# Kernel optimization log

Measured on AMD Instinct MI355X. Metric: run time of the kernel, lower is better.

## Reference

```python
import jax, jax.numpy as jnp
import numpy as np

B, T, C, H = 4, 2048, 1024, 16
D = C // H  # head_dim = 64
ROPE_BASE = 10000.0


def _rope_cos_sin(T, D, dtype):
    # inv_freq: (D/2,), freqs: (T, D/2) -> cos/sin tiled to (T, D)
    inv_freq = 1.0 / (ROPE_BASE ** (jnp.arange(0, D, 2, dtype=jnp.float32) / D))
    freqs = jnp.arange(T, dtype=jnp.float32)[:, None] * inv_freq[None, :]
    emb = jnp.concatenate([freqs, freqs], axis=-1)  # (T, D)
    return jnp.cos(emb).astype(dtype), jnp.sin(emb).astype(dtype)


def _rotate_half(x):
    x1, x2 = jnp.split(x, 2, axis=-1)
    return jnp.concatenate([-x2, x1], axis=-1)


def setup_inputs() -> dict:
    key = jax.random.key(0)
    k1, k2, k3 = jax.random.split(key, 3)
    x = jax.random.normal(k1, (B, T, C), dtype=jnp.float32)
    W_qkv = jax.random.normal(k2, (C, 3 * C), dtype=jnp.float32) * (C ** -0.5)
    b_qkv = jnp.zeros((3 * C,), dtype=jnp.float32)
    W_out = jax.random.normal(k3, (C, C), dtype=jnp.float32) * (C ** -0.5)
    b_out = jnp.zeros((C,), dtype=jnp.float32)
    return {"x": x, "W_qkv": W_qkv, "b_qkv": b_qkv, "W_out": W_out, "b_out": b_out}


def reference(x, W_qkv, b_qkv, W_out, b_out):
    Bx, Tx, Cx = x.shape
    qkv = x @ W_qkv + b_qkv                                   # (B, T, 3C)
    qkv = qkv.reshape(Bx, Tx, 3, H, D).transpose(2, 0, 3, 1, 4)  # (3, B, H, T, D)
    q, k, v = qkv[0], qkv[1], qkv[2]

    cos, sin = _rope_cos_sin(Tx, D, x.dtype)                  # (T, D) each
    q = q * cos + _rotate_half(q) * sin
    k = k * cos + _rotate_half(k) * sin

    # NOTE: original code has no 1/sqrt(D) scaling — faithful reproduction.
    att = jnp.einsum('bhtd,bhsd->bhts', q, k)                 # (B, H, T, T)
    causal = jnp.tril(jnp.ones((Tx, Tx), dtype=bool))
    att = jnp.where(causal[None, None, :, :], att, -jnp.inf)
    att = jax.nn.softmax(att, axis=-1)
    y = jnp.einsum('bhts,bhsd->bhtd', att, v)                 # (B, H, T, D)
    y = y.transpose(0, 2, 1, 3).reshape(Bx, Tx, Cx)
    return y @ W_out + b_out
```

## Files before the change

kernel.cpp:

```cpp
#include <hip/hip_runtime.h>
#include <math.h>

#define NB    4
#define T_SEQ 2048
#define CDIM  1024
#define NH    16
#define DH    64
#define NQKV  3072

typedef short bf16x8 __attribute__((ext_vector_type(8)));
typedef float f32x4  __attribute__((ext_vector_type(4)));

#define GLOBAL_AS __attribute__((address_space(1)))
#define LDS_AS    __attribute__((address_space(3)))

__device__ __forceinline__ void async16(const void* g, void* l) {
  __builtin_amdgcn_global_load_lds((const GLOBAL_AS void*)g, (LDS_AS void*)l, 16, 0, 0);
}

__device__ __forceinline__ unsigned short f2bf(float f) {
  unsigned u = __float_as_uint(f);
  unsigned r = u + 0x7FFF + ((u >> 16) & 1);
  return (unsigned short)(r >> 16);
}

#define SWZ8(row, c) ((((row) << 3) | ((c) ^ ((row) & 7))) << 3)

#define BARRIER()  asm volatile("s_barrier" ::: "memory")
#define VMCNT(n)   asm volatile("s_waitcnt vmcnt(" #n ")" ::: "memory")

__global__ __launch_bounds__(256) void rope_table(float2* __restrict__ tab) {
  int i = blockIdx.x * 256 + threadIdx.x;
  int t = i >> 5, d = i & 31;
  float inv = expf((float)d * -0.28782313662425572f);
  float s, c;
  sincosf((float)t * inv, &s, &c);
  tab[i] = make_float2(c, s);
}

__global__ __launch_bounds__(256) void convert_bf16(
    const float* __restrict__ in, unsigned short* __restrict__ out, int n4) {
  int i = blockIdx.x * 256 + threadIdx.x;
  if (i >= n4) return;
  float4 v = ((const float4*)in)[i];
  ushort4 o;
  o.x = f2bf(v.x); o.y = f2bf(v.y); o.z = f2bf(v.z); o.w = f2bf(v.w);
  ((ushort4*)out)[i] = o;
}

__global__ __launch_bounds__(256) void transpose_to_bf16(
    const float* __restrict__ in, unsigned short* __restrict__ out, int K, int N) {
  __shared__ float tile[32][33];
  int n0 = blockIdx.x << 5, k0 = blockIdx.y << 5;
  int r  = threadIdx.x >> 3;
  int c4 = (threadIdx.x & 7) << 2;
  float4 v = *(const float4*)&in[(size_t)(k0 + r) * N + n0 + c4];
  tile[r][c4 + 0] = v.x; tile[r][c4 + 1] = v.y;
  tile[r][c4 + 2] = v.z; tile[r][c4 + 3] = v.w;
  __syncthreads();
  ushort4 o;
  o.x = f2bf(tile[c4 + 0][r]); o.y = f2bf(tile[c4 + 1][r]);
  o.z = f2bf(tile[c4 + 2][r]); o.w = f2bf(tile[c4 + 3][r]);
  *(ushort4*)&out[(size_t)(n0 + r) * K + k0 + c4] = o;
}

__global__ __launch_bounds__(256) void transpose_v(
    const unsigned short* __restrict__ v, unsigned short* __restrict__ vt) {
  __shared__ unsigned short tile[64][65];
  int bh = blockIdx.y;
  int t0 = blockIdx.x << 6;
  size_t ib = (size_t)bh * (T_SEQ * DH);
  int tid = threadIdx.x;
#pragma unroll
  for (int u = 0; u < 2; ++u) {
    int f = u * 256 + tid;
    int tr = f >> 3, c = f & 7;
    bf16x8 val = *(const bf16x8*)&v[ib + (size_t)(t0 + tr) * DH + c * 8];
#pragma unroll
    for (int j = 0; j < 8; ++j) tile[tr][c * 8 + j] = (unsigned short)val[j];
  }
  __syncthreads();
#pragma unroll
  for (int u = 0; u < 2; ++u) {
    int f = u * 256 + tid;
    int d = f >> 3, c = f & 7;
    bf16x8 o;
#pragma unroll
    for (int j = 0; j < 8; ++j) o[j] = (short)tile[c * 8 + j][d];
    *(bf16x8*)&vt[ib + (size_t)d * T_SEQ + t0 + c * 8] = o;
  }
}

#define STAGE(kt, b)                                                          \
  { const unsigned short* sa_ = aSrc + (kt) * 64;                             \
    const unsigned short* sb_ = bSrc + (kt) * 64;                             \
    async16(sa_,          &As[b][d0]);                                        \
    async16(sa_ + 65536,  &As[b][d0 + 4096]);                                 \
    async16(sb_,          &Bs[b][d0]);                                        \
    async16(sb_ + 65536,  &Bs[b][d0 + 4096]);                                 \
    async16(sb_ + 131072, &Bs[b][d0 + 8192]);                                 \
    async16(sb_ + 196608, &Bs[b][d0 + 12288]); }

#define GEMM_PIPE(Aptr, Btptr)                                                \
  int tid = threadIdx.x;                                                      \
  int wave = tid >> 6, lane = tid & 63;                                       \
  int wm = wave >> 2, wn = wave & 3;                                          \
  int col = lane & 15, quad = lane >> 4;                                      \
  int srow = tid >> 3;                                                        \
  int schunk = (tid & 7) ^ (srow & 7);                                        \
  const unsigned short* aSrc = &Aptr[(size_t)(m0 + srow) * CDIM + schunk * 8];\
  const unsigned short* bSrc = &Btptr[(size_t)(n0 + srow) * CDIM + schunk * 8];\
  int d0 = wave * 512;      \
  f32x4 acc[4][4];                                                            \
  _Pragma("unroll") for (int mt = 0; mt < 4; ++mt)                            \
  _Pragma("unroll") for (int nt = 0; nt < 4; ++nt)                            \
    acc[mt][nt] = (f32x4){0.f, 0.f, 0.f, 0.f};                                \
  STAGE(0, 0)                                                                 \
  STAGE(1, 1)                                                                 \
  _Pragma("unroll")                                                           \
  for (int t = 0; t < 16; ++t) {                                              \
    if (t < 15) { VMCNT(6); } else { VMCNT(0); }                              \
    BARRIER();                                                                \
    if (t + 2 < 16) STAGE(t + 2, (t + 2) % 3)                                 \
    const short* A_ = As[t % 3];                                              \
    const short* B_ = Bs[t % 3];                                              \
    _Pragma("unroll") for (int ks = 0; ks < 2; ++ks) {                        \
      bf16x8 af[4], bfr[4];                                                   \
      _Pragma("unroll") for (int mt = 0; mt < 4; ++mt)                        \
        af[mt] = *(const bf16x8*)&A_[SWZ8(wm * 64 + mt * 16 + col,            \
                                          ks * 4 + quad)];                    \
      _Pragma("unroll") for (int nt = 0; nt < 4; ++nt)                        \
        bfr[nt] = *(const bf16x8*)&B_[SWZ8(wn * 64 + nt * 16 + col,           \
                                           ks * 4 + quad)];                   \
      __builtin_amdgcn_s_setprio(1);                                          \
      _Pragma("unroll") for (int mt = 0; mt < 4; ++mt)                        \
        _Pragma("unroll") for (int nt = 0; nt < 4; ++nt)                      \
          acc[mt][nt] = __builtin_amdgcn_mfma_f32_16x16x32_bf16(              \
              af[mt], bfr[nt], acc[mt][nt], 0, 0, 0);                         \
      __builtin_amdgcn_s_setprio(0);                                          \
    }                                                                         \
  }

__global__ __launch_bounds__(512, 2) void gemm_qkv_mfma(
    const unsigned short* __restrict__ A, const unsigned short* __restrict__ Bt,
    const float* __restrict__ bias, const float2* __restrict__ rope,
    unsigned short* __restrict__ qb, unsigned short* __restrict__ kb,
    unsigned short* __restrict__ vb) {
  __shared__ short As[3][128 * 64];
  __shared__ short Bs[3][256 * 64];
  int orig = blockIdx.x;
  int wg = (orig & 7) * 96 + (orig >> 3);
  int m0 = (wg / 12) << 7, n0 = (wg % 12) << 8;
  GEMM_PIPE(A, Bt)
  int nn = n0 + wn * 64;
  int which = nn >> 10;
  int h = (nn >> 6) & 15;
  unsigned short* dst = (which == 0) ? qb : ((which == 1) ? kb : vb);
  float bv[4];
#pragma unroll
  for (int nt = 0; nt < 4; ++nt) bv[nt] = bias[nn + nt * 16 + col];
  if (which < 2) {
#pragma unroll
    for (int mt = 0; mt < 4; ++mt) {
#pragma unroll
      for (int r = 0; r < 4; ++r) {
        int m = m0 + wm * 64 + mt * 16 + quad * 4 + r;
        int bidx = m >> 11, t = m & 2047;
        float x0 = acc[mt][0][r] + bv[0];
        float x1 = acc[mt][1][r] + bv[1];
        float x2 = acc[mt][2][r] + bv[2];
        float x3 = acc[mt][3][r] + bv[3];
        float2 cs0 = rope[(t << 5) + col];
        float2 cs1 = rope[(t << 5) + col + 16];
        size_t ro = (((size_t)bidx * NH + h) * T_SEQ + t) * DH;
        dst[ro + col]      = f2bf(x0 * cs0.x - x2 * cs0.y);
        dst[ro + col + 16] = f2bf(x1 * cs1.x - x3 * cs1.y);
        dst[ro + col + 32] = f2bf(x2 * cs0.x + x0 * cs0.y);
        dst[ro + col + 48] = f2bf(x3 * cs1.x + x1 * cs1.y);
      }
    }
  } else {
#pragma unroll
    for (int mt = 0; mt < 4; ++mt) {
#pragma unroll
      for (int r = 0; r < 4; ++r) {
        int m = m0 + wm * 64 + mt * 16 + quad * 4 + r;
        int bidx = m >> 11, t = m & 2047;
        size_t ro = (((size_t)bidx * NH + h) * T_SEQ + t) * DH;
        dst[ro + col]      = f2bf(acc[mt][0][r] + bv[0]);
        dst[ro + col + 16] = f2bf(acc[mt][1][r] + bv[1]);
        dst[ro + col + 32] = f2bf(acc[mt][2][r] + bv[2]);
        dst[ro + col + 48] = f2bf(acc[mt][3][r] + bv[3]);
      }
    }
  }
}

__global__ __launch_bounds__(512, 2) void gemm_out_mfma(
    const unsigned short* __restrict__ A, const unsigned short* __restrict__ Bt,
    const float* __restrict__ bias, float* __restrict__ out) {
  __shared__ short As[3][128 * 64];
  __shared__ short Bs[3][256 * 64];
  int orig = blockIdx.x;
  int wg = (orig & 7) * 32 + (orig >> 3);
  int m0 = (wg >> 2) << 7, n0 = (wg & 3) << 8;
  GEMM_PIPE(A, Bt)
#pragma unroll
  for (int nt = 0; nt < 4; ++nt) {
    int n = n0 + wn * 64 + nt * 16 + col;
    float bv = bias[n];
#pragma unroll
    for (int mt = 0; mt < 4; ++mt) {
#pragma unroll
      for (int r = 0; r < 4; ++r) {
        int m = m0 + wm * 64 + mt * 16 + quad * 4 + r;
        out[(size_t)m * CDIM + n] = acc[mt][nt][r] + bv;
      }
    }
  }
}

__global__ __launch_bounds__(256) void attn_mfma(
    const unsigned short* __restrict__ qg, const unsigned short* __restrict__ kg,
    const unsigned short* __restrict__ vtg, unsigned short* __restrict__ yb) {
  __shared__ short Ks[64 * 64];
  __shared__ short Vts[64 * 64];
  __shared__ short Ps[4][32 * 64];
  int tid = threadIdx.x;
  int wave = tid >> 6, lane = tid & 63;
  int col = lane & 15, quad = lane >> 4;
  int bh = blockIdx.x;
  int qblk = 15 - (int)blockIdx.y;
  int qb0 = qblk << 7;
  size_t base = (size_t)bh * (T_SEQ * DH);

  bf16x8 qreg[2][2];
#pragma unroll
  for (int nt = 0; nt < 2; ++nt)
#pragma unroll
    for (int kc = 0; kc < 2; ++kc)
      qreg[nt][kc] = *(const bf16x8*)&qg[base +
          (size_t)(qb0 + wave * 32 + nt * 16 + col) * DH + kc * 32 + quad * 8];

  bf16x8 ones;
#pragma unroll
  for (int j = 0; j < 8; ++j) ones[j] = (short)0x3F80;

  f32x4 oc[2][4], lsum[2];
#pragma unroll
  for (int mq = 0; mq < 2; ++mq) {
    lsum[mq] = (f32x4){0.f, 0.f, 0.f, 0.f};
#pragma unroll
    for (int dt = 0; dt < 4; ++dt) oc[mq][dt] = (f32x4){0.f, 0.f, 0.f, 0.f};
  }

  int qlo = qb0 + wave * 32;
  int qhi = qlo + 31;
  int nkb = (qblk << 1) + 2;
  for (int kb = 0; kb < nkb; ++kb) {
    int s0 = kb << 6;
    __syncthreads();
#pragma unroll
    for (int u = 0; u < 2; ++u) {
      int ff = u * 256 + wave * 64 + lane;
      int row = ff >> 3, cl = ff & 7;
      int cg = cl ^ (row & 7);
      async16(&kg[base + (size_t)(s0 + row) * DH + cg * 8],
              &Ks[(u * 256 + wave * 64) * 8]);
      async16(&vtg[base + (size_t)row * T_SEQ + s0 + cg * 8],
              &Vts[(u * 256 + wave * 64) * 8]);
    }
    __syncthreads();
    if (s0 > qhi) continue;

    f32x4 sc[4][2];
#pragma unroll
    for (int mf = 0; mf < 4; ++mf)
#pragma unroll
      for (int nt = 0; nt < 2; ++nt) sc[mf][nt] = (f32x4){0.f, 0.f, 0.f, 0.f};
#pragma unroll
    for (int kc = 0; kc < 2; ++kc) {
#pragma unroll
      for (int mf = 0; mf < 4; ++mf) {
        bf16x8 ak = *(const bf16x8*)&Ks[SWZ8(mf * 16 + col, kc * 4 + quad)];
        sc[mf][0] = __builtin_amdgcn_mfma_f32_16x16x32_bf16(ak, qreg[0][kc], sc[mf][0], 0, 0, 0);
        sc[mf][1] = __builtin_amdgcn_mfma_f32_16x16x32_bf16(ak, qreg[1][kc], sc[mf][1], 0, 0, 0);
      }
    }

    if (s0 + 63 > qlo) {
#pragma unroll
      for (int mf = 0; mf < 4; ++mf) {
        int kbase = s0 + mf * 16 + quad * 4;
#pragma unroll
        for (int nt = 0; nt < 2; ++nt) {
          int qq = qlo + nt * 16 + col;
#pragma unroll
          for (int r = 0; r < 4; ++r)
            if (kbase + r > qq) sc[mf][nt][r] = -3.0e38f;
        }
      }
    }

#pragma unroll
    for (int nt = 0; nt < 2; ++nt) {
      int row = nt * 16 + col;
      int rb = row << 6;
      int sw = row & 7;
#pragma unroll
      for (int mf = 0; mf < 4; ++mf) {
        float p0 = __expf(sc[mf][nt][0]);
        float p1 = __expf(sc[mf][nt][1]);
        float p2 = __expf(sc[mf][nt][2]);
        float p3 = __expf(sc[mf][nt][3]);
        unsigned w0, w1;
        asm("v_cvt_pk_bf16_f32 %0, %1, %2" : "=v"(w0) : "v"(p0), "v"(p1));
        asm("v_cvt_pk_bf16_f32 %0, %1, %2" : "=v"(w1) : "v"(p2), "v"(p3));
        int chunk = (mf << 1) | (quad >> 1);
        int off = rb + (((chunk ^ sw) << 3) | ((quad & 1) << 2));
        *(uint2*)&Ps[wave][off] = make_uint2(w0, w1);
      }
    }

#pragma unroll
    for (int kc = 0; kc < 2; ++kc) {
      bf16x8 ap0 = *(const bf16x8*)&Ps[wave][SWZ8(col,      kc * 4 + quad)];
      bf16x8 ap1 = *(const bf16x8*)&Ps[wave][SWZ8(16 + col, kc * 4 + quad)];
      lsum[0] = __builtin_amdgcn_mfma_f32_16x16x32_bf16(ap0, ones, lsum[0], 0, 0, 0);
      lsum[1] = __builtin_amdgcn_mfma_f32_16x16x32_bf16(ap1, ones, lsum[1], 0, 0, 0);
#pragma unroll
      for (int dt = 0; dt < 4; ++dt) {
        bf16x8 vb = *(const bf16x8*)&Vts[SWZ8(dt * 16 + col, kc * 4 + quad)];
        oc[0][dt] = __builtin_amdgcn_mfma_f32_16x16x32_bf16(ap0, vb, oc[0][dt], 0, 0, 0);
        oc[1][dt] = __builtin_amdgcn_mfma_f32_16x16x32_bf16(ap1, vb, oc[1][dt], 0, 0, 0);
      }
    }
  }

  int b = bh >> 4, h = bh & 15;
#pragma unroll
  for (int mq = 0; mq < 2; ++mq)
#pragma unroll
    for (int dt = 0; dt < 4; ++dt) {
      int d = dt * 16 + col;
#pragma unroll
      for (int r = 0; r < 4; ++r) {
        int t = qb0 + wave * 32 + mq * 16 + quad * 4 + r;
        yb[(((size_t)b * T_SEQ + t) * NH + h) * DH + d] =
            f2bf(oc[mq][dt][r] / lsum[mq][r]);
      }
    }
}

extern "C" void kernel_launch(void* const* d_in, const int* in_sizes, int n_in,
                              void* d_out, int out_size, void* d_ws, size_t ws_size,
                              hipStream_t stream) {
  const float* x     = (const float*)d_in[0];
  const float* W_qkv = (const float*)d_in[1];
  const float* b_qkv = (const float*)d_in[2];
  const float* W_out = (const float*)d_in[3];
  const float* b_out = (const float*)d_in[4];
  float* out = (float*)d_out;

  const size_t per = (size_t)NB * NH * T_SEQ * DH;
  unsigned short* xb  = (unsigned short*)d_ws;
  unsigned short* qb  = xb + per;
  unsigned short* kbf = qb + per;
  unsigned short* vbf = kbf + per;
  unsigned short* vtb = vbf + per;
  unsigned short* yb  = vtb + per;
  unsigned short* wqt = yb + per;
  unsigned short* wot = wqt + (size_t)NQKV * CDIM;
  float2* rope = (float2*)(wot + (size_t)CDIM * CDIM);

  rope_table<<<256, 256, 0, stream>>>(rope);
  convert_bf16<<<(int)(per / 4 / 256), 256, 0, stream>>>(x, xb, (int)(per / 4));
  transpose_to_bf16<<<dim3(NQKV / 32, CDIM / 32), 256, 0, stream>>>(W_qkv, wqt, CDIM, NQKV);
  transpose_to_bf16<<<dim3(CDIM / 32, CDIM / 32), 256, 0, stream>>>(W_out, wot, CDIM, CDIM);
  gemm_qkv_mfma<<<768, 512, 0, stream>>>(xb, wqt, b_qkv, rope, qb, kbf, vbf);
  transpose_v<<<dim3(T_SEQ / 64, NB * NH), 256, 0, stream>>>(vbf, vtb);
  attn_mfma<<<dim3(NB * NH, T_SEQ / 128), 256, 0, stream>>>(qb, kbf, vtb, yb);
  gemm_out_mfma<<<256, 512, 0, stream>>>(yb, wot, b_out, out);
}
```

Baseline: 255.1 us.

## Fuse prep kernels into one launch and load two KV tiles per barrier round

Merges the rope table, x-to-bf16 conversion and both weight transposes into a single kernel that dispatches on block index, removing three launches. In attention, each loop round now async-loads two 64-key K/V tiles into doubled LDS buffers and processes both between one pair of barriers, halving barrier count. The cost is double LDS for K/V, which can lower occupancy, plus some wasted loads when the second tile lies beyond the causal range.

```diff
diff --git a/kernel.cpp b/kernel.cpp
--- a/kernel.cpp
+++ b/kernel.cpp
@@ -29,31 +29,12 @@
 #define BARRIER()  asm volatile("s_barrier" ::: "memory")
 #define VMCNT(n)   asm volatile("s_waitcnt vmcnt(" #n ")" ::: "memory")
 
-__global__ __launch_bounds__(256) void rope_table(float2* __restrict__ tab) {
-  int i = blockIdx.x * 256 + threadIdx.x;
-  int t = i >> 5, d = i & 31;
-  float inv = expf((float)d * -0.28782313662425572f);
-  float s, c;
-  sincosf((float)t * inv, &s, &c);
-  tab[i] = make_float2(c, s);
-}
-
-__global__ __launch_bounds__(256) void convert_bf16(
-    const float* __restrict__ in, unsigned short* __restrict__ out, int n4) {
-  int i = blockIdx.x * 256 + threadIdx.x;
-  if (i >= n4) return;
-  float4 v = ((const float4*)in)[i];
-  ushort4 o;
-  o.x = f2bf(v.x); o.y = f2bf(v.y); o.z = f2bf(v.z); o.w = f2bf(v.w);
-  ((ushort4*)out)[i] = o;
-}
-
-__global__ __launch_bounds__(256) void transpose_to_bf16(
-    const float* __restrict__ in, unsigned short* __restrict__ out, int K, int N) {
-  __shared__ float tile[32][33];
-  int n0 = blockIdx.x << 5, k0 = blockIdx.y << 5;
-  int r  = threadIdx.x >> 3;
-  int c4 = (threadIdx.x & 7) << 2;
+__device__ __forceinline__ void transpose_tile32(
+    const float* __restrict__ in, unsigned short* __restrict__ out,
+    int K, int N, int bx, int by, float (*tile)[33], int tid) {
+  int n0 = bx << 5, k0 = by << 5;
+  int r  = tid >> 3;
+  int c4 = (tid & 7) << 2;
   float4 v = *(const float4*)&in[(size_t)(k0 + r) * N + n0 + c4];
   tile[r][c4 + 0] = v.x; tile[r][c4 + 1] = v.y;
   tile[r][c4 + 2] = v.z; tile[r][c4 + 3] = v.w;
@@ -62,6 +43,36 @@
   o.x = f2bf(tile[c4 + 0][r]); o.y = f2bf(tile[c4 + 1][r]);
   o.z = f2bf(tile[c4 + 2][r]); o.w = f2bf(tile[c4 + 3][r]);
   *(ushort4*)&out[(size_t)(n0 + r) * K + k0 + c4] = o;
+}
+
+__global__ __launch_bounds__(256) void prep_fused(
+    const float* __restrict__ x, unsigned short* __restrict__ xb,
+    const float* __restrict__ W_qkv, unsigned short* __restrict__ wqt,
+    const float* __restrict__ W_out, unsigned short* __restrict__ wot,
+    float2* __restrict__ rope) {
+  __shared__ float tile[32][33];
+  int blk = blockIdx.x;
+  int tid = threadIdx.x;
+  if (blk < 8192) {
+    int i = blk * 256 + tid;
+    float4 v = ((const float4*)x)[i];
+    ushort4 o;
+    o.x = f2bf(v.x); o.y = f2bf(v.y); o.z = f2bf(v.z); o.w = f2bf(v.w);
+    ((ushort4*)xb)[i] = o;
+  } else if (blk < 11264) {
+    int local = blk - 8192;
+    transpose_tile32(W_qkv, wqt, CDIM, NQKV, local % 96, local / 96, tile, tid);
+  } else if (blk < 12288) {
+    int local = blk - 11264;
+    transpose_tile32(W_out, wot, CDIM, CDIM, local & 31, local >> 5, tile, tid);
+  } else {
+    int i = (blk - 12288) * 256 + tid;
+    int t = i >> 5, d = i & 31;
+    float inv = expf((float)d * -0.28782313662425572f);
+    float s, c;
+    sincosf((float)t * inv, &s, &c);
+    rope[i] = make_float2(c, s);
+  }
 }
 
 __global__ __launch_bounds__(256) void transpose_v(
@@ -223,8 +234,8 @@
 __global__ __launch_bounds__(256) void attn_mfma(
     const unsigned short* __restrict__ qg, const unsigned short* __restrict__ kg,
     const unsigned short* __restrict__ vtg, unsigned short* __restrict__ yb) {
-  __shared__ short Ks[64 * 64];
-  __shared__ short Vts[64 * 64];
+  __shared__ short Ks[2][64 * 64];
+  __shared__ short Vts[2][64 * 64];
   __shared__ short Ps[4][32 * 64];
   int tid = threadIdx.x;
   int wave = tid >> 6, lane = tid & 63;
@@ -256,83 +267,94 @@
 
   int qlo = qb0 + wave * 32;
   int qhi = qlo + 31;
-  int nkb = (qblk << 1) + 2;
-  for (int kb = 0; kb < nkb; ++kb) {
-    int s0 = kb << 6;
+  int nrounds = qblk + 1;
+  for (int rr = 0; rr < nrounds; ++rr) {
     __syncthreads();
 #pragma unroll
-    for (int u = 0; u < 2; ++u) {
-      int ff = u * 256 + wave * 64 + lane;
-      int row = ff >> 3, cl = ff & 7;
-      int cg = cl ^ (row & 7);
-      async16(&kg[base + (size_t)(s0 + row) * DH + cg * 8],
-              &Ks[(u * 256 + wave * 64) * 8]);
-      async16(&vtg[base + (size_t)row * T_SEQ + s0 + cg * 8],
-              &Vts[(u * 256 + wave * 64) * 8]);
+    for (int v = 0; v < 2; ++v) {
+      int s_ = (rr * 2 + v) << 6;
+#pragma unroll
+      for (int u = 0; u < 2; ++u) {
+        int ff = u * 256 + wave * 64 + lane;
+        int row = ff >> 3, cl = ff & 7;
+        int cg = cl ^ (row & 7);
+        async16(&kg[base + (size_t)(s_ + row) * DH + cg * 8],
+                &Ks[v][(u * 256 + wave * 64) * 8]);
+        async16(&vtg[base + (size_t)row * T_SEQ + s_ + cg * 8],
+                &Vts[v][(u * 256 + wave * 64) * 8]);
+      }
     }
     __syncthreads();
-    if (s0 > qhi) continue;
-
-    f32x4 sc[4][2];
-#pragma unroll
-    for (int mf = 0; mf < 4; ++mf)
-#pragma unroll
-      for (int nt = 0; nt < 2; ++nt) sc[mf][nt] = (f32x4){0.f, 0.f, 0.f, 0.f};
-#pragma unroll
-    for (int kc = 0; kc < 2; ++kc) {
-#pragma unroll
-      for (int mf = 0; mf < 4; ++mf) {
-        bf16x8 ak = *(const bf16x8*)&Ks[SWZ8(mf * 16 + col, kc * 4 + quad)];
-        sc[mf][0] = __builtin_amdgcn_mfma_f32_16x16x32_bf16(ak, qreg[0][kc], sc[mf][0], 0, 0, 0);
-        sc[mf][1] = __builtin_amdgcn_mfma_f32_16x16x32_bf16(ak, qreg[1][kc], sc[mf][1], 0, 0, 0);
-      }
-    }
-
-    if (s0 + 63 > qlo) {
-#pragma unroll
-      for (int mf = 0; mf < 4; ++mf) {
-        int kbase = s0 + mf * 16 + quad * 4;
-#pragma unroll
-        for (int nt = 0; nt < 2; ++nt) {
-          int qq = qlo + nt * 16 + col;
-#pragma unroll
-          for (int r = 0; r < 4; ++r)
-            if (kbase + r > qq) sc[mf][nt][r] = -3.0e38f;
+
+#pragma unroll
+    for (int v = 0; v < 2; ++v) {
+      int kb = rr * 2 + v;
+      int s0 = kb << 6;
+      if (s0 > qhi) continue;
+      const short* K_ = Ks[v];
+      const short* V_ = Vts[v];
+
+      f32x4 sc[4][2];
+#pragma unroll
+      for (int mf = 0; mf < 4; ++mf)
+#pragma unroll
+        for (int nt = 0; nt < 2; ++nt) sc[mf][nt] = (f32x4){0.f, 0.f, 0.f, 0.f};
+#pragma unroll
+      for (int kc = 0; kc < 2; ++kc) {
+#pragma unroll
+        for (int mf = 0; mf < 4; ++mf) {
+          bf16x8 ak = *(const bf16x8*)&K_[SWZ8(mf * 16 + col, kc * 4 + quad)];
+          sc[mf][0] = __builtin_amdgcn_mfma_f32_16x16x32_bf16(ak, qreg[0][kc], sc[mf][0], 0, 0, 0);
+          sc[mf][1] = __builtin_amdgcn_mfma_f32_16x16x32_bf16(ak, qreg[1][kc], sc[mf][1], 0, 0, 0);
         }
       }
-    }
-
-#pragma unroll
-    for (int nt = 0; nt < 2; ++nt) {
-      int row = nt * 16 + col;
-      int rb = row << 6;
-      int sw = row & 7;
-#pragma unroll
-      for (int mf = 0; mf < 4; ++mf) {
-        float p0 = __expf(sc[mf][nt][0]);
-        float p1 = __expf(sc[mf][nt][1]);
-        float p2 = __expf(sc[mf][nt][2]);
-        float p3 = __expf(sc[mf][nt][3]);
-        unsigned w0, w1;
-        asm("v_cvt_pk_bf16_f32 %0, %1, %2" : "=v"(w0) : "v"(p0), "v"(p1));
-        asm("v_cvt_pk_bf16_f32 %0, %1, %2" : "=v"(w1) : "v"(p2), "v"(p3));
-        int chunk = (mf << 1) | (quad >> 1);
-        int off = rb + (((chunk ^ sw) << 3) | ((quad & 1) << 2));
-        *(uint2*)&Ps[wave][off] = make_uint2(w0, w1);
-      }
-    }
-
-#pragma unroll
-    for (int kc = 0; kc < 2; ++kc) {
-      bf16x8 ap0 = *(const bf16x8*)&Ps[wave][SWZ8(col,      kc * 4 + quad)];
-      bf16x8 ap1 = *(const bf16x8*)&Ps[wave][SWZ8(16 + col, kc * 4 + quad)];
-      lsum[0] = __builtin_amdgcn_mfma_f32_16x16x32_bf16(ap0, ones, lsum[0], 0, 0, 0);
-      lsum[1] = __builtin_amdgcn_mfma_f32_16x16x32_bf16(ap1, ones, lsum[1], 0, 0, 0);
-#pragma unroll
-      for (int dt = 0; dt < 4; ++dt) {
-        bf16x8 vb = *(const bf16x8*)&Vts[SWZ8(dt * 16 + col, kc * 4 + quad)];
-        oc[0][dt] = __builtin_amdgcn_mfma_f32_16x16x32_bf16(ap0, vb, oc[0][dt], 0, 0, 0);
-        oc[1][dt] = __builtin_amdgcn_mfma_f32_16x16x32_bf16(ap1, vb, oc[1][dt], 0, 0, 0);
+
+      if (s0 + 63 > qlo) {
+#pragma unroll
+        for (int mf = 0; mf < 4; ++mf) {
+          int kbase = s0 + mf * 16 + quad * 4;
+#pragma unroll
+          for (int nt = 0; nt < 2; ++nt) {
+            int qq = qlo + nt * 16 + col;
+#pragma unroll
+            for (int r = 0; r < 4; ++r)
+              if (kbase + r > qq) sc[mf][nt][r] = -3.0e38f;
+          }
+        }
+      }
+
+#pragma unroll
+      for (int nt = 0; nt < 2; ++nt) {
+        int row = nt * 16 + col;
+        int rb = row << 6;
+        int sw = row & 7;
+#pragma unroll
+        for (int mf = 0; mf < 4; ++mf) {
+          float p0 = __expf(sc[mf][nt][0]);
+          float p1 = __expf(sc[mf][nt][1]);
+          float p2 = __expf(sc[mf][nt][2]);
+          float p3 = __expf(sc[mf][nt][3]);
+          unsigned w0, w1;
+          asm("v_cvt_pk_bf16_f32 %0, %1, %2" : "=v"(w0) : "v"(p0), "v"(p1));
+          asm("v_cvt_pk_bf16_f32 %0, %1, %2" : "=v"(w1) : "v"(p2), "v"(p3));
+          int chunk = (mf << 1) | (quad >> 1);
+          int off = rb + (((chunk ^ sw) << 3) | ((quad & 1) << 2));
+          *(uint2*)&Ps[wave][off] = make_uint2(w0, w1);
+        }
+      }
+
+#pragma unroll
+      for (int kc = 0; kc < 2; ++kc) {
+        bf16x8 ap0 = *(const bf16x8*)&Ps[wave][SWZ8(col,      kc * 4 + quad)];
+        bf16x8 ap1 = *(const bf16x8*)&Ps[wave][SWZ8(16 + col, kc * 4 + quad)];
+        lsum[0] = __builtin_amdgcn_mfma_f32_16x16x32_bf16(ap0, ones, lsum[0], 0, 0, 0);
+        lsum[1] = __builtin_amdgcn_mfma_f32_16x16x32_bf16(ap1, ones, lsum[1], 0, 0, 0);
+#pragma unroll
+        for (int dt = 0; dt < 4; ++dt) {
+          bf16x8 vb = *(const bf16x8*)&V_[SWZ8(dt * 16 + col, kc * 4 + quad)];
+          oc[0][dt] = __builtin_amdgcn_mfma_f32_16x16x32_bf16(ap0, vb, oc[0][dt], 0, 0, 0);
+          oc[1][dt] = __builtin_amdgcn_mfma_f32_16x16x32_bf16(ap1, vb, oc[1][dt], 0, 0, 0);
+        }
       }
     }
   }
@@ -373,10 +395,7 @@
   unsigned short* wot = wqt + (size_t)NQKV * CDIM;
   float2* rope = (float2*)(wot + (size_t)CDIM * CDIM);
 
-  rope_table<<<256, 256, 0, stream>>>(rope);
-  convert_bf16<<<(int)(per / 4 / 256), 256, 0, stream>>>(x, xb, (int)(per / 4));
-  transpose_to_bf16<<<dim3(NQKV / 32, CDIM / 32), 256, 0, stream>>>(W_qkv, wqt, CDIM, NQKV);
-  transpose_to_bf16<<<dim3(CDIM / 32, CDIM / 32), 256, 0, stream>>>(W_out, wot, CDIM, CDIM);
+  prep_fused<<<12544, 256, 0, stream>>>(x, xb, W_qkv, wqt, W_out, wot, rope);
   gemm_qkv_mfma<<<768, 512, 0, stream>>>(xb, wqt, b_qkv, rope, qb, kbf, vbf);
   transpose_v<<<dim3(T_SEQ / 64, NB * NH), 256, 0, stream>>>(vbf, vtb);
   attn_mfma<<<dim3(NB * NH, T_SEQ / 128), 256, 0, stream>>>(qb, kbf, vtb, yb);
```

Measured after the change: 247.3 us. 3.0% less time.
